# Performance work log

Measured on AMD Instinct MI355X. Metric: run time of the kernel, lower is better.

## Reference

```python
import jax, jax.numpy as jnp
import numpy as np

N = 32768
E = 524288
NFEAT = 256
NHID = 256
NUM_HEADS = 4
HEAD_DIM = NHID // NUM_HEADS
NLAYER = 2
EPS = 1e-5


def setup_inputs():
    keys = iter(jax.random.split(jax.random.key(0), 64))

    def nrm(shape, scale=0.05):
        return jax.random.normal(next(keys), shape, dtype=jnp.float32) * scale

    inp = {
        "x": jax.random.normal(next(keys), (N, NFEAT), dtype=jnp.float32),
        "edge_src": jax.random.randint(next(keys), (E,), 0, N),
        "edge_dst": jax.random.randint(next(keys), (E,), 0, N),
        "edge_attr": jax.random.uniform(next(keys), (E,), dtype=jnp.float32) * 0.1,
        "num_graphs": 64,
    }
    for i in range(NLAYER):
        fin = NFEAT if i == 0 else NHID
        inp["conv_w%d" % i] = nrm((fin, NHID))
        inp["bn_g%d" % i] = jnp.ones((NHID,), jnp.float32)
        inp["bn_b%d" % i] = jnp.zeros((NHID,), jnp.float32)
        inp["bn_m%d" % i] = nrm((NHID,), 0.1)
        inp["bn_v%d" % i] = 1.0 + jax.random.uniform(next(keys), (NHID,), dtype=jnp.float32) * 0.1
        inp["attn_in_w%d" % i] = nrm((3 * NHID, NHID))
        inp["attn_in_b%d" % i] = jnp.zeros((3 * NHID,), jnp.float32)
        inp["attn_out_w%d" % i] = nrm((NHID, NHID))
        inp["attn_out_b%d" % i] = jnp.zeros((NHID,), jnp.float32)
        inp["ln_g%d" % i] = jnp.ones((NHID,), jnp.float32)
        inp["ln_b%d" % i] = jnp.zeros((NHID,), jnp.float32)
    inp["score_w"] = nrm((1, NHID))
    inp["score_b"] = jnp.zeros((1,), jnp.float32)
    return inp


def _mha(xb, iw, ib, ow, ob):
    # torch.nn.MultiheadAttention (batch_first), all graphs same length so
    # key_padding_mask is all-False (no masked positions).
    B, S, H = xb.shape
    q, k, v = jnp.split(xb @ iw.T + ib, 3, axis=-1)
    heads = lambda t: t.reshape(B, S, NUM_HEADS, HEAD_DIM).transpose(0, 2, 1, 3)
    q, k, v = heads(q), heads(k), heads(v)
    scale = jnp.float32(1.0 / np.sqrt(HEAD_DIM))
    att = jax.nn.softmax(jnp.einsum("bhqd,bhkd->bhqk", q, k) * scale, axis=-1)
    o = jnp.einsum("bhqk,bhkd->bhqd", att, v).transpose(0, 2, 1, 3).reshape(B, S, H)
    return o @ ow.T + ob


def _forward(x, edge_attr, params, edge_src, edge_dst, num_graphs):
    n = x.shape[0]
    B = num_graphs
    S = n // B  # equal-sized graphs -> max_nodes == S, pad is a no-op
    h = x
    for i, (cw, bng, bnb, bnm, bnv, iw, ib, ow, ob, lg, lb) in enumerate(params):
        # DIGCNConv: out[dst] += edge_attr * (x @ W)[src]
        conv = jax.ops.segment_sum(edge_attr[:, None] * (h @ cw)[edge_src], edge_dst, num_segments=n)
        # BatchNorm1d (eval mode, running stats)
        conv = (conv - bnm) * jax.lax.rsqrt(bnv + EPS) * bng + bnb
        # ragged gather -> pad/stack -> MHA -> unpad (equal graph sizes => reshape)
        attended = _mha(conv.reshape(B, S, NHID), iw, ib, ow, ob).reshape(n, NHID)
        y = conv + attended
        mu = jnp.mean(y, axis=-1, keepdims=True)
        var = jnp.mean((y - mu) ** 2, axis=-1, keepdims=True)
        h = (y - mu) * jax.lax.rsqrt(var + EPS) * lg + lb  # LayerNorm
        if i < NLAYER - 1:
            h = jax.nn.relu(h)
    return h


def reference(x, edge_src, edge_dst, edge_attr, num_graphs,
              conv_w0, bn_g0, bn_b0, bn_m0, bn_v0, attn_in_w0, attn_in_b0, attn_out_w0, attn_out_b0, ln_g0, ln_b0,
              conv_w1, bn_g1, bn_b1, bn_m1, bn_v1, attn_in_w1, attn_in_b1, attn_out_w1, attn_out_b1, ln_g1, ln_b1,
              score_w, score_b):
    params = [
        (conv_w0, bn_g0, bn_b0, bn_m0, bn_v0, attn_in_w0, attn_in_b0, attn_out_w0, attn_out_b0, ln_g0, ln_b0),
        (conv_w1, bn_g1, bn_b1, bn_m1, bn_v1, attn_in_w1, attn_in_b1, attn_out_w1, attn_out_b1, ln_g1, ln_b1),
    ]
    h = _forward(x, edge_attr, params, edge_src, edge_dst, num_graphs)
    scores = (h @ score_w.T + score_b)[:, 0]
    # emb_list / score_list are per-graph views of these flat arrays
    return h, scores
```

## Files before the change

kernel.cpp:

```cpp
#include <hip/hip_runtime.h>
#include <hip/hip_bf16.h>
#include <math.h>

#define N_NODES 32768
#define E_EDGES 524288
#define NHID    256
#define HEAD_DIM 64
#define SEQ     512
#define EPS_LN  1e-5f
#define SM_SCALE 0.18033688011112042f

typedef __hip_bfloat16 bf16;
typedef __attribute__((ext_vector_type(8))) short short8;
typedef __attribute__((ext_vector_type(4))) float floatx4;
static const size_t NH = (size_t)N_NODES * NHID;

__device__ __forceinline__ void unpack2(unsigned int u, float& lo, float& hi) {
    union { float f; unsigned int i; } a, b;
    a.i = u << 16; b.i = u & 0xffff0000u;
    lo = a.f; hi = b.f;
}

__device__ __forceinline__ void* swzp(void* base, int row, int col) {
    return (char*)base + (((row << 7) + (col << 1)) ^ ((row & 7) << 4));
}

__device__ __forceinline__ void gload16(const bf16* g, void* lds) {
    __builtin_amdgcn_global_load_lds((const __attribute__((address_space(1))) void*)g,
                                     (__attribute__((address_space(3))) void*)lds, 16, 0, 0);
}

__global__ __launch_bounds__(256) void k_stage2(
    const float* __restrict__ cw0, const float* __restrict__ g0, const float* __restrict__ b0,
    const float* __restrict__ m0, const float* __restrict__ v0, const float* __restrict__ iw0,
    const float* __restrict__ ow0,
    const float* __restrict__ cw1, const float* __restrict__ g1, const float* __restrict__ b1,
    const float* __restrict__ m1, const float* __restrict__ v1, const float* __restrict__ iw1,
    const float* __restrict__ ow1,
    bf16* __restrict__ iwb0, bf16* __restrict__ owb0, bf16* __restrict__ cwT0,
    float* __restrict__ bns0, float* __restrict__ bnt0,
    bf16* __restrict__ iwb1, bf16* __restrict__ owb1, bf16* __restrict__ cwT1,
    float* __restrict__ bns1, float* __restrict__ bnt1,
    const float* __restrict__ x, bf16* __restrict__ xb) {
    const int blk = blockIdx.x;
    const int tid = threadIdx.x;
    if (blk >= 1026) {
        size_t i = (size_t)((blk - 1026) * 256 + tid) * 4;
        const float4 v = *(const float4*)(x + i);
        __align__(8) bf16 t4[4];
        t4[0] = __float2bfloat16(v.x);
        t4[1] = __float2bfloat16(v.y);
        t4[2] = __float2bfloat16(v.z);
        t4[3] = __float2bfloat16(v.w);
        *(uint2*)(xb + i) = *(uint2*)t4;
        return;
    }
    const int L = (blk >= 513);
    const int b2 = L ? blk - 513 : blk;
    const float* cw = L ? cw1 : cw0;
    const float* bng = L ? g1 : g0;
    const float* bnb = L ? b1 : b0;
    const float* bnm = L ? m1 : m0;
    const float* bnv = L ? v1 : v0;
    const float* iw = L ? iw1 : iw0;
    const float* ow = L ? ow1 : ow0;
    bf16* iwb = L ? iwb1 : iwb0;
    bf16* owb = L ? owb1 : owb0;
    bf16* cwT = L ? cwT1 : cwT0;
    float* bns = L ? bns1 : bns0;
    float* bnt = L ? bnt1 : bnt0;
    if (b2 < 256) {
        const float* src = (b2 < 192) ? iw : ow;
        bf16* dst = (b2 < 192) ? iwb : owb;
        size_t i = (size_t)((b2 < 192 ? b2 : b2 - 192) * 256 + tid) * 4;
        const float4 v = *(const float4*)(src + i);
        __align__(8) bf16 t4[4];
        t4[0] = __float2bfloat16(v.x);
        t4[1] = __float2bfloat16(v.y);
        t4[2] = __float2bfloat16(v.z);
        t4[3] = __float2bfloat16(v.w);
        *(uint2*)(dst + i) = *(uint2*)t4;
    } else if (b2 < 512) {
        const int k = b2 - 256;
        cwT[(size_t)tid * 256 + k] = __float2bfloat16(cw[(size_t)k * 256 + tid]);
    } else {
        float sv = bng[tid] * rsqrtf(bnv[tid] + EPS_LN);
        bns[tid] = sv;
        bnt[tid] = bnb[tid] - bnm[tid] * sv;
    }
}

__global__ void k_hist(const int* __restrict__ edst, int* __restrict__ counts) {
    int e = blockIdx.x * 256 + threadIdx.x;
    atomicAdd(&counts[edst[e]], 1);
}

__global__ __launch_bounds__(256) void k_scan(const int* __restrict__ counts,
                                              int* __restrict__ offsets,
                                              int* __restrict__ cursor) {
    __shared__ int sums[256];
    const int tid = threadIdx.x;
    const int base = tid * 128;
    int s = 0;
    for (int i = 0; i < 128; ++i) s += counts[base + i];
    sums[tid] = s;
    __syncthreads();
    for (int off = 1; off < 256; off <<= 1) {
        int v = (tid >= off) ? sums[tid - off] : 0;
        __syncthreads();
        sums[tid] += v;
        __syncthreads();
    }
    int run = (tid == 0) ? 0 : sums[tid - 1];
    for (int i = 0; i < 128; ++i) {
        int c = counts[base + i];
        offsets[base + i] = run;
        cursor[base + i] = run;
        run += c;
    }
    if (tid == 255) offsets[32768] = run;
}

__global__ void k_fill(const int* __restrict__ esrc, const int* __restrict__ edst,
                       const float* __restrict__ eattr, int* __restrict__ cursor,
                       int* __restrict__ srcp, float* __restrict__ attrp) {
    int e = blockIdx.x * 256 + threadIdx.x;
    int d = edst[e];
    int slot = atomicAdd(&cursor[d], 1);
    srcp[slot] = esrc[e];
    attrp[slot] = eattr[e];
}

__global__ __launch_bounds__(256) void k_gather(const bf16* __restrict__ t,
                                                const int* __restrict__ offsets,
                                                const int* __restrict__ srcp,
                                                const float* __restrict__ attrp,
                                                const float* __restrict__ bns,
                                                const float* __restrict__ bnt,
                                                bf16* __restrict__ conv) {
    const int node = (blockIdx.x * 256 + threadIdx.x) >> 6;
    const int lane = threadIdx.x & 63;
    const int half = lane >> 5;
    const int l32 = lane & 31;
    const int start = offsets[node];
    const int end = offsets[node + 1];
    float a[8];
#pragma unroll
    for (int i = 0; i < 8; ++i) a[i] = 0.f;
    for (int c0 = start; c0 < end; c0 += 64) {
        const int n = min(64, end - c0);
        int sidx = 0;
        float sa = 0.f;
        if (lane < n) {
            sidx = srcp[c0 + lane];
            sa = attrp[c0 + lane];
        }
        int s = __shfl(sidx, half, 64);
        float aw = __shfl(sa, half, 64);
        uint4 u = *(const uint4*)(t + (size_t)s * 256 + l32 * 8);
        for (int j = 0; j < n; j += 2) {
            const int e2 = (j + 2 + half) & 63;
            const int s2 = __shfl(sidx, e2, 64);
            const float aw2 = __shfl(sa, e2, 64);
            const uint4 u2 = *(const uint4*)(t + (size_t)s2 * 256 + l32 * 8);
            float v0, v1, v2, v3, v4, v5, v6, v7;
            unpack2(u.x, v0, v1);
            unpack2(u.y, v2, v3);
            unpack2(u.z, v4, v5);
            unpack2(u.w, v6, v7);
            a[0] = fmaf(aw, v0, a[0]);
            a[1] = fmaf(aw, v1, a[1]);
            a[2] = fmaf(aw, v2, a[2]);
            a[3] = fmaf(aw, v3, a[3]);
            a[4] = fmaf(aw, v4, a[4]);
            a[5] = fmaf(aw, v5, a[5]);
            a[6] = fmaf(aw, v6, a[6]);
            a[7] = fmaf(aw, v7, a[7]);
            u = u2;
            aw = aw2;
        }
    }
#pragma unroll
    for (int i = 0; i < 8; ++i) a[i] += __shfl_xor(a[i], 32, 64);
    if (half == 0) {
        const int c = l32 * 8;
        const float4 s0 = *(const float4*)(bns + c);
        const float4 s1 = *(const float4*)(bns + c + 4);
        const float4 t0 = *(const float4*)(bnt + c);
        const float4 t1 = *(const float4*)(bnt + c + 4);
        __align__(16) bf16 tmp[8];
        tmp[0] = __float2bfloat16(fmaf(a[0], s0.x, t0.x));
        tmp[1] = __float2bfloat16(fmaf(a[1], s0.y, t0.y));
        tmp[2] = __float2bfloat16(fmaf(a[2], s0.z, t0.z));
        tmp[3] = __float2bfloat16(fmaf(a[3], s0.w, t0.w));
        tmp[4] = __float2bfloat16(fmaf(a[4], s1.x, t1.x));
        tmp[5] = __float2bfloat16(fmaf(a[5], s1.y, t1.y));
        tmp[6] = __float2bfloat16(fmaf(a[6], s1.z, t1.z));
        tmp[7] = __float2bfloat16(fmaf(a[7], s1.w, t1.w));
        *(uint4*)(conv + (size_t)node * 256 + c) = *(uint4*)tmp;
    }
}

__global__ __launch_bounds__(256) void k_gemm(const bf16* __restrict__ A,
                                              const bf16* __restrict__ WT,
                                              const float* __restrict__ bias,
                                              bf16* __restrict__ C, bf16* __restrict__ VT,
                                              int ldc, int qkvmode) {
    __shared__ __align__(16) short As[2][128 * 64];
    __shared__ __align__(16) short Bs[2][128 * 64];
    const int tid = threadIdx.x;
    const int bm = blockIdx.x * 128;
    const int bn = blockIdx.y * 128;
    const int wid = tid >> 6;
    const int lane = tid & 63;
    const int wr = (wid >> 1) * 64;
    const int wc = (wid & 1) * 64;
    const int quad = lane >> 4;
    const int l16 = lane & 15;

    floatx4 acc[4][4];
#pragma unroll
    for (int mi = 0; mi < 4; ++mi)
#pragma unroll
        for (int ni = 0; ni < 4; ++ni)
            acc[mi][ni] = (floatx4){0.f, 0.f, 0.f, 0.f};

    auto STAGE = [&](int ks, int bf) {
#pragma unroll
        for (int t = 0; t < 4; ++t) {
            const int p = ((t * 4 + wid) << 10) + (lane << 4);
            const int row = p >> 7;
            const int cb = (p & 127) ^ ((row & 7) << 4);
            gload16(A + (size_t)(bm + row) * 256 + ks * 64 + (cb >> 1),
                    (char*)&As[bf][0] + ((t * 4 + wid) << 10));
            gload16(WT + (size_t)(bn + row) * 256 + ks * 64 + (cb >> 1),
                    (char*)&Bs[bf][0] + ((t * 4 + wid) << 10));
        }
    };

    STAGE(0, 0);
    __syncthreads();
    for (int t = 0; t < 4; ++t) {
        const int buf = t & 1;
        if (t < 3) STAGE(t + 1, buf ^ 1);
#pragma unroll
        for (int kk = 0; kk < 2; ++kk) {
            const int kcol = kk * 32 + quad * 8;
            short8 af[4], bfr[4];
#pragma unroll
            for (int mi = 0; mi < 4; ++mi)
                af[mi] = *(const short8*)swzp(&As[buf][0], wr + mi * 16 + l16, kcol);
#pragma unroll
            for (int ni = 0; ni < 4; ++ni)
                bfr[ni] = *(const short8*)swzp(&Bs[buf][0], wc + ni * 16 + l16, kcol);
#pragma unroll
            for (int mi = 0; mi < 4; ++mi)
#pragma unroll
                for (int ni = 0; ni < 4; ++ni)
                    acc[mi][ni] = __builtin_amdgcn_mfma_f32_16x16x32_bf16(af[mi], bfr[ni],
                                                                          acc[mi][ni], 0, 0, 0);
        }
        __syncthreads();
    }
    const float cs = (qkvmode && bn < 256) ? SM_SCALE : 1.0f;
    const bool vpath = (qkvmode && bn >= 512);
#pragma unroll
    for (int ni = 0; ni < 4; ++ni) {
        const int gc = bn + wc + ni * 16 + l16;
        const float bv = bias ? bias[gc] : 0.f;
#pragma unroll
        for (int mi = 0; mi < 4; ++mi) {
            const int gr = bm + wr + mi * 16 + quad * 4;
            if (vpath) {
                const int head = (gc - 512) >> 6;
                const int d = (gc - 512) & 63;
                const int bg = gr >> 9;
                const int sl = gr & 511;
                __align__(8) bf16 t4[4];
#pragma unroll
                for (int r = 0; r < 4; ++r) t4[r] = __float2bfloat16(acc[mi][ni][r] + bv);
                *(uint2*)(VT + (((size_t)((bg * 4 + head) * 64 + d)) << 9) + sl) = *(uint2*)t4;
            } else {
#pragma unroll
                for (int r = 0; r < 4; ++r)
                    C[(size_t)(gr + r) * ldc + gc] = __float2bfloat16((acc[mi][ni][r] + bv) * cs);
            }
        }
    }
}

__global__ __launch_bounds__(256) void k_gemmln(const bf16* __restrict__ A,
                                                const bf16* __restrict__ WT,
                                                const float* __restrict__ bias,
                                                const bf16* __restrict__ conv,
                                                const float* __restrict__ lg,
                                                const float* __restrict__ lb,
                                                bf16* __restrict__ h,
                                                const float* __restrict__ sw,
                                                const float* __restrict__ sb,
                                                float* __restrict__ out, int mode) {
    __shared__ __align__(16) short As[2][64 * 64];
    __shared__ __align__(16) short Bs[2][256 * 64];
    const int tid = threadIdx.x;
    const int bm = blockIdx.x * 64;
    const int wid = tid >> 6;
    const int lane = tid & 63;
    const int wc = wid * 64;
    const int quad = lane >> 4;
    const int l16 = lane & 15;

    floatx4 acc[4][4];
#pragma unroll
    for (int mi = 0; mi < 4; ++mi)
#pragma unroll
        for (int ni = 0; ni < 4; ++ni)
            acc[mi][ni] = (floatx4){0.f, 0.f, 0.f, 0.f};

    auto STAGE = [&](int ks, int bf) {
#pragma unroll
        for (int t = 0; t < 2; ++t) {
            const int base = (t * 4 + wid) << 10;
            const int p = base + (lane << 4);
            const int row = p >> 7;
            const int cb = (p & 127) ^ ((row & 7) << 4);
            gload16(A + (size_t)(bm + row) * 256 + ks * 64 + (cb >> 1),
                    (char*)&As[bf][0] + base);
        }
#pragma unroll
        for (int t = 0; t < 8; ++t) {
            const int base = (t * 4 + wid) << 10;
            const int p = base + (lane << 4);
            const int row = p >> 7;
            const int cb = (p & 127) ^ ((row & 7) << 4);
            gload16(WT + (size_t)row * 256 + ks * 64 + (cb >> 1), (char*)&Bs[bf][0] + base);
        }
    };

    STAGE(0, 0);
    __syncthreads();
    for (int t = 0; t < 4; ++t) {
        const int buf = t & 1;
        if (t < 3) STAGE(t + 1, buf ^ 1);
#pragma unroll
        for (int kk = 0; kk < 2; ++kk) {
            const int kcol = kk * 32 + quad * 8;
            short8 af[4], bfr[4];
#pragma unroll
            for (int mi = 0; mi < 4; ++mi)
                af[mi] = *(const short8*)swzp(&As[buf][0], mi * 16 + l16, kcol);
#pragma unroll
            for (int ni = 0; ni < 4; ++ni)
                bfr[ni] = *(const short8*)swzp(&Bs[buf][0], wc + ni * 16 + l16, kcol);
#pragma unroll
            for (int mi = 0; mi < 4; ++mi)
#pragma unroll
                for (int ni = 0; ni < 4; ++ni)
                    acc[mi][ni] = __builtin_amdgcn_mfma_f32_16x16x32_bf16(af[mi], bfr[ni],
                                                                          acc[mi][ni], 0, 0, 0);
        }
        __syncthreads();
    }

#pragma unroll
    for (int ni = 0; ni < 4; ++ni) {
        const int gc = wc + ni * 16 + l16;
        const float bv = bias[gc];
#pragma unroll
        for (int mi = 0; mi < 4; ++mi) {
            const int gr = bm + mi * 16 + quad * 4;
#pragma unroll
            for (int r = 0; r < 4; ++r)
                acc[mi][ni][r] += bv + __bfloat162float(conv[(size_t)(gr + r) * 256 + gc]);
        }
    }

    float* red = (float*)&As[0][0];
    float* red2 = red + 256;
    float* red3 = red2 + 256;
    float* redb = red3 + 256;

#pragma unroll
    for (int mi = 0; mi < 4; ++mi)
#pragma unroll
        for (int r = 0; r < 4; ++r) {
            float s1 = acc[mi][0][r] + acc[mi][1][r] + acc[mi][2][r] + acc[mi][3][r];
            s1 += __shfl_xor(s1, 1, 64);
            s1 += __shfl_xor(s1, 2, 64);
            s1 += __shfl_xor(s1, 4, 64);
            s1 += __shfl_xor(s1, 8, 64);
            if (l16 == 0) red[(mi * 16 + quad * 4 + r) * 4 + wid] = s1;
        }
    float lg4[4], lb4[4], w34[4];
#pragma unroll
    for (int ni = 0; ni < 4; ++ni) {
        const int gc = wc + ni * 16 + l16;
        lg4[ni] = lg[gc];
        lb4[ni] = lb[gc];
        w34[ni] = mode ? lg4[ni] * sw[gc] : 0.f;
    }
    if (mode) {
        float pb = 0.f;
#pragma unroll
        for (int ni = 0; ni < 4; ++ni) pb += lb4[ni] * sw[wc + ni * 16 + l16];
        pb += __shfl_xor(pb, 1, 64);
        pb += __shfl_xor(pb, 2, 64);
        pb += __shfl_xor(pb, 4, 64);
        pb += __shfl_xor(pb, 8, 64);
        if (lane == 0) redb[wid] = pb;
    }
    __syncthreads();

    float mu_[4][4];
#pragma unroll
    for (int mi = 0; mi < 4; ++mi)
#pragma unroll
        for (int r = 0; r < 4; ++r) {
            const int row = mi * 16 + quad * 4 + r;
            const float mu = (red[row * 4 + 0] + red[row * 4 + 1] + red[row * 4 + 2] +
                              red[row * 4 + 3]) * (1.f / 256.f);
            mu_[mi][r] = mu;
            float s2 = 0.f, s3 = 0.f;
#pragma unroll
            for (int ni = 0; ni < 4; ++ni) {
                const float d = acc[mi][ni][r] - mu;
                s2 += d * d;
                s3 += d * w34[ni];
            }
            s2 += __shfl_xor(s2, 1, 64);
            s2 += __shfl_xor(s2, 2, 64);
            s2 += __shfl_xor(s2, 4, 64);
            s2 += __shfl_xor(s2, 8, 64);
            if (mode) {
                s3 += __shfl_xor(s3, 1, 64);
                s3 += __shfl_xor(s3, 2, 64);
                s3 += __shfl_xor(s3, 4, 64);
                s3 += __shfl_xor(s3, 8, 64);
            }
            if (l16 == 0) {
                red2[row * 4 + wid] = s2;
                if (mode) red3[row * 4 + wid] = s3;
            }
        }
    __syncthreads();

    const float B0 = mode ? (redb[0] + redb[1] + redb[2] + redb[3] + sb[0]) : 0.f;
#pragma unroll
    for (int mi = 0; mi < 4; ++mi)
#pragma unroll
        for (int r = 0; r < 4; ++r) {
            const int row = mi * 16 + quad * 4 + r;
            const int gr = bm + row;
            const float mu = mu_[mi][r];
            const float var = (red2[row * 4 + 0] + red2[row * 4 + 1] + red2[row * 4 + 2] +
                               red2[row * 4 + 3]) * (1.f / 256.f);
            const float rstd = rsqrtf(var + EPS_LN);
            if (!mode) {
#pragma unroll
                for (int ni = 0; ni < 4; ++ni) {
                    const int gc = wc + ni * 16 + l16;
                    const float o = fmaf((acc[mi][ni][r] - mu) * rstd, lg4[ni], lb4[ni]);
                    h[(size_t)gr * 256 + gc] = __float2bfloat16(fmaxf(o, 0.f));
                }
            } else {
#pragma unroll
                for (int ni = 0; ni < 4; ++ni) {
                    const int gc = wc + ni * 16 + l16;
                    out[(size_t)gr * 256 + gc] =
                        fmaf((acc[mi][ni][r] - mu) * rstd, lg4[ni], lb4[ni]);
                }
                if (wid == 0 && l16 == 0) {
                    const float S3 = red3[row * 4 + 0] + red3[row * 4 + 1] +
                                     red3[row * 4 + 2] + red3[row * 4 + 3];
                    out[(size_t)N_NODES * 256 + gr] = fmaf(rstd, S3, B0);
                }
            }
        }
}

__global__ __launch_bounds__(256) void k_fattn(const bf16* __restrict__ qkv,
                                               const bf16* __restrict__ vtb,
                                               bf16* __restrict__ ctx) {
    const int bid = ((blockIdx.x & 7) << 8) | (blockIdx.x >> 3);
    const int qt = bid & 7;
    const int head = (bid >> 3) & 3;
    const int b = bid >> 5;
    const int tid = threadIdx.x;
    const int wave = tid >> 6;
    const int lane = tid & 63;
    const int quad = lane >> 4;
    const int l16 = lane & 15;
    const int qrow0 = b * SEQ + qt * 64 + wave * 16;

    __shared__ __align__(16) short Ks[2][64 * 64];
    __shared__ __align__(16) short Vt[2][64 * 64];
    __shared__ __align__(16) short Ps[4][16 * 64];

    const bf16* kbase = qkv + (size_t)(b * SEQ) * 768 + 256 + head * HEAD_DIM;
    const bf16* vbase = vtb + (size_t)((b * 4 + head) * 64) * 512;
    const int pbase = (wave << 10) + (lane << 4);

    short8 af_q[2];
    {
        const bf16* qp = qkv + (size_t)(qrow0 + l16) * 768 + head * HEAD_DIM + quad * 8;
        af_q[0] = *(const short8*)(qp);
        af_q[1] = *(const short8*)(qp + 32);
    }
    short8 ones;
#pragma unroll
    for (int j = 0; j < 8; ++j) ones[j] = (short)0x3F80;

    floatx4 acc[5];
#pragma unroll
    for (int nt = 0; nt < 5; ++nt) acc[nt] = (floatx4){0.f, 0.f, 0.f, 0.f};

    auto STAGE = [&](int kt2, int bf) {
#pragma unroll
        for (int i = 0; i < 2; ++i) {
            const int p = (i << 12) + pbase;
            const int row = p >> 7;
            const int cb = (p & 127) ^ ((row & 7) << 4);
            gload16(kbase + (size_t)(kt2 * 64 + row) * 768 + (cb >> 1),
                    (char*)Ks[bf] + (i << 12) + (wave << 10));
            gload16(vbase + (size_t)row * 512 + kt2 * 64 + (cb >> 1),
                    (char*)Vt[bf] + (i << 12) + (wave << 10));
        }
    };

    STAGE(0, 0);
    __syncthreads();

    for (int kt = 0; kt < 8; ++kt) {
        const int buf = kt & 1;
        if (kt < 7) STAGE(kt + 1, buf ^ 1);

        floatx4 sf[4];
#pragma unroll
        for (int f = 0; f < 4; ++f) {
            const short8 bk0 = *(const short8*)swzp(Ks[buf], f * 16 + l16, quad * 8);
            const short8 bk1 = *(const short8*)swzp(Ks[buf], f * 16 + l16, 32 + quad * 8);
            sf[f] = __builtin_amdgcn_mfma_f32_16x16x32_bf16(af_q[0], bk0,
                                                            (floatx4){0.f, 0.f, 0.f, 0.f}, 0, 0, 0);
            sf[f] = __builtin_amdgcn_mfma_f32_16x16x32_bf16(af_q[1], bk1, sf[f], 0, 0, 0);
        }

        bf16* psb = (bf16*)&Ps[wave][0];
#pragma unroll
        for (int r = 0; r < 4; ++r) {
            const float p0 = exp2f(fminf(sf[0][r], 80.f));
            const float p1 = exp2f(fminf(sf[1][r], 80.f));
            const float p2 = exp2f(fminf(sf[2][r], 80.f));
            const float p3 = exp2f(fminf(sf[3][r], 80.f));
            const int qr = quad * 4 + r;
            *(bf16*)swzp(psb, qr, l16)      = __float2bfloat16(p0);
            *(bf16*)swzp(psb, qr, 16 + l16) = __float2bfloat16(p1);
            *(bf16*)swzp(psb, qr, 32 + l16) = __float2bfloat16(p2);
            *(bf16*)swzp(psb, qr, 48 + l16) = __float2bfloat16(p3);
        }

#pragma unroll
        for (int c2 = 0; c2 < 2; ++c2) {
            const short8 ap = *(const short8*)swzp(psb, l16, c2 * 32 + quad * 8);
#pragma unroll
            for (int nt = 0; nt < 4; ++nt) {
                const short8 bv = *(const short8*)swzp(Vt[buf], nt * 16 + l16, c2 * 32 + quad * 8);
                acc[nt] = __builtin_amdgcn_mfma_f32_16x16x32_bf16(ap, bv, acc[nt], 0, 0, 0);
            }
            acc[4] = __builtin_amdgcn_mfma_f32_16x16x32_bf16(ap, ones, acc[4], 0, 0, 0);
        }
        __syncthreads();
    }

#pragma unroll
    for (int r = 0; r < 4; ++r) {
        const float inv = 1.f / acc[4][r];
        bf16* op = ctx + (size_t)(qrow0 + quad * 4 + r) * 256 + head * HEAD_DIM + l16;
        op[0]  = __float2bfloat16(acc[0][r] * inv);
        op[16] = __float2bfloat16(acc[1][r] * inv);
        op[32] = __float2bfloat16(acc[2][r] * inv);
        op[48] = __float2bfloat16(acc[3][r] * inv);
    }
}

extern "C" void kernel_launch(void* const* d_in, const int* in_sizes, int n_in,
                              void* d_out, int out_size, void* d_ws, size_t ws_size,
                              hipStream_t stream) {
    if (ws_size < (size_t)100663296) return;

    const float* x     = (const float*)d_in[0];
    const int*   esrc  = (const int*)d_in[1];
    const int*   edst  = (const int*)d_in[2];
    const float* eattr = (const float*)d_in[3];

    bf16* convb = (bf16*)d_ws;
    bf16* qkvb  = convb + NH;
    bf16* tb    = qkvb + 3 * NH;
    bf16* vtb   = tb + NH;
    bf16* xb  = qkvb;
    bf16* hb  = qkvb + NH;

    char* scr = (char*)d_out;
    const size_t LBYTES = 393216 + 131072 + 131072 + 2048;
    int*   counts  = (int*)(scr + 2 * LBYTES);
    int*   offsets = counts + 32768;
    int*   cursor  = offsets + 32769;
    int*   srcp    = cursor + 32768;
    float* attrp   = (float*)(srcp + E_EDGES);

    (void)hipMemsetAsync(counts, 0, 32768 * sizeof(int), stream);
    k_hist<<<E_EDGES / 256, 256, 0, stream>>>(edst, counts);
    k_scan<<<1, 256, 0, stream>>>(counts, offsets, cursor);
    k_fill<<<E_EDGES / 256, 256, 0, stream>>>(esrc, edst, eattr, cursor, srcp, attrp);

    bf16*  iwb[2];
    bf16*  owb[2];
    bf16*  cwT[2];
    float* bns[2];
    float* bnt[2];
    for (int L = 0; L < 2; ++L) {
        char* base = scr + (size_t)L * LBYTES;
        iwb[L] = (bf16*)base;
        owb[L] = iwb[L] + 196608;
        cwT[L] = owb[L] + 65536;
        bns[L] = (float*)(cwT[L] + 65536);
        bnt[L] = bns[L] + 256;
    }
    k_stage2<<<9218, 256, 0, stream>>>(
        (const float*)d_in[5], (const float*)d_in[6], (const float*)d_in[7],
        (const float*)d_in[8], (const float*)d_in[9], (const float*)d_in[10],
        (const float*)d_in[12],
        (const float*)d_in[16], (const float*)d_in[17], (const float*)d_in[18],
        (const float*)d_in[19], (const float*)d_in[20], (const float*)d_in[21],
        (const float*)d_in[23],
        iwb[0], owb[0], cwT[0], bns[0], bnt[0],
        iwb[1], owb[1], cwT[1], bns[1], bnt[1],
        x, xb);

    for (int L = 0; L < 2; ++L) {
        int bi = 5 + L * 11;
        const float* ib = (const float*)d_in[bi + 6];
        const float* ob = (const float*)d_in[bi + 8];

        k_gemm<<<dim3(256, 2), 256, 0, stream>>>(L == 0 ? xb : hb, cwT[L], nullptr, tb,
                                                 nullptr, 256, 0);
        k_gather<<<8192, 256, 0, stream>>>(tb, offsets, srcp, attrp, bns[L], bnt[L], convb);
        k_gemm<<<dim3(256, 6), 256, 0, stream>>>(convb, iwb[L], ib, qkvb, vtb, 768, 1);
        k_fattn<<<2048, 256, 0, stream>>>(qkvb, vtb, tb);
        k_gemmln<<<512, 256, 0, stream>>>(tb, owb[L], ob, convb, (const float*)d_in[bi + 9],
                                          (const float*)d_in[bi + 10], hb,
                                          (const float*)d_in[27], (const float*)d_in[28],
                                          (float*)d_out, L);
    }
}
```

Measured before the change: 495.3 us.

## Preload full weight matrix into LDS and reuse row GEMM for conv projection

The GEMM+LayerNorm kernel becomes a general row-block GEMM that loads the entire 256x256 bf16 weight matrix into four LDS buffers up front, then streams only the A tiles double-buffered. It adds a plain-output mode, which replaces the previous tiled k_gemm for the conv weight projection. For the second layer, a small copy kernel first moves the output-projection weights into a scratch buffer. The aim is to stop reloading weight tiles on every k-step. The cost is a large LDS footprint that limits occupancy to about one block per CU, the loss of overlap for weight loads, and an extra kernel launch.

Measured after the change: 528.7 us. +6.7%, slower.

```diff
diff --git a/kernel.cpp b/kernel.cpp
--- a/kernel.cpp
+++ b/kernel.cpp
@@ -289,18 +289,19 @@
     }
 }
 
-__global__ __launch_bounds__(256) void k_gemmln(const bf16* __restrict__ A,
-                                                const bf16* __restrict__ WT,
-                                                const float* __restrict__ bias,
-                                                const bf16* __restrict__ conv,
-                                                const float* __restrict__ lg,
-                                                const float* __restrict__ lb,
-                                                bf16* __restrict__ h,
-                                                const float* __restrict__ sw,
-                                                const float* __restrict__ sb,
-                                                float* __restrict__ out, int mode) {
+__global__ __launch_bounds__(256) void k_rgemm(const bf16* __restrict__ A,
+                                               const bf16* __restrict__ WT,
+                                               const float* __restrict__ bias,
+                                               bf16* __restrict__ C, int ldc,
+                                               const bf16* __restrict__ conv,
+                                               const float* __restrict__ lg,
+                                               const float* __restrict__ lb,
+                                               bf16* __restrict__ h,
+                                               const float* __restrict__ sw,
+                                               const float* __restrict__ sb,
+                                               float* __restrict__ out, int mode) {
+    __shared__ __align__(16) short Bs[4][256 * 64];
     __shared__ __align__(16) short As[2][64 * 64];
-    __shared__ __align__(16) short Bs[2][256 * 64];
     const int tid = threadIdx.x;
     const int bm = blockIdx.x * 64;
     const int wid = tid >> 6;
@@ -316,7 +317,17 @@
         for (int ni = 0; ni < 4; ++ni)
             acc[mi][ni] = (floatx4){0.f, 0.f, 0.f, 0.f};
 
-    auto STAGE = [&](int ks, int bf) {
+#pragma unroll
+    for (int ks = 0; ks < 4; ++ks)
+#pragma unroll
+        for (int t = 0; t < 8; ++t) {
+            const int base = (t * 4 + wid) << 10;
+            const int p = base + (lane << 4);
+            const int row = p >> 7;
+            const int cb = (p & 127) ^ ((row & 7) << 4);
+            gload16(WT + (size_t)row * 256 + ks * 64 + (cb >> 1), (char*)&Bs[ks][0] + base);
+        }
+    auto STAGE_A = [&](int ks, int bf) {
 #pragma unroll
         for (int t = 0; t < 2; ++t) {
             const int base = (t * 4 + wid) << 10;
@@ -326,21 +337,13 @@
             gload16(A + (size_t)(bm + row) * 256 + ks * 64 + (cb >> 1),
                     (char*)&As[bf][0] + base);
         }
-#pragma unroll
-        for (int t = 0; t < 8; ++t) {
-            const int base = (t * 4 + wid) << 10;
-            const int p = base + (lane << 4);
-            const int row = p >> 7;
-            const int cb = (p & 127) ^ ((row & 7) << 4);
-            gload16(WT + (size_t)row * 256 + ks * 64 + (cb >> 1), (char*)&Bs[bf][0] + base);
-        }
     };
-
-    STAGE(0, 0);
+    STAGE_A(0, 0);
     __syncthreads();
-    for (int t = 0; t < 4; ++t) {
-        const int buf = t & 1;
-        if (t < 3) STAGE(t + 1, buf ^ 1);
+
+    for (int ks = 0; ks < 4; ++ks) {
+        const int buf = ks & 1;
+        if (ks < 3) STAGE_A(ks + 1, buf ^ 1);
 #pragma unroll
         for (int kk = 0; kk < 2; ++kk) {
             const int kcol = kk * 32 + quad * 8;
@@ -350,7 +353,7 @@
                 af[mi] = *(const short8*)swzp(&As[buf][0], mi * 16 + l16, kcol);
 #pragma unroll
             for (int ni = 0; ni < 4; ++ni)
-                bfr[ni] = *(const short8*)swzp(&Bs[buf][0], wc + ni * 16 + l16, kcol);
+                bfr[ni] = *(const short8*)swzp(&Bs[ks][0], wc + ni * 16 + l16, kcol);
 #pragma unroll
             for (int mi = 0; mi < 4; ++mi)
 #pragma unroll
@@ -361,6 +364,22 @@
         __syncthreads();
     }
 
+    if (mode == 0) {
+#pragma unroll
+        for (int ni = 0; ni < 4; ++ni) {
+            const int gc = wc + ni * 16 + l16;
+            const float bv = bias ? bias[gc] : 0.f;
+#pragma unroll
+            for (int mi = 0; mi < 4; ++mi) {
+                const int gr = bm + mi * 16 + quad * 4;
+#pragma unroll
+                for (int r = 0; r < 4; ++r)
+                    C[(size_t)(gr + r) * ldc + gc] = __float2bfloat16(acc[mi][ni][r] + bv);
+            }
+        }
+        return;
+    }
+
 #pragma unroll
     for (int ni = 0; ni < 4; ++ni) {
         const int gc = wc + ni * 16 + l16;
@@ -373,7 +392,7 @@
                 acc[mi][ni][r] += bv + __bfloat162float(conv[(size_t)(gr + r) * 256 + gc]);
         }
     }
-
+    const int sc = (mode == 2);
     float* red = (float*)&As[0][0];
     float* red2 = red + 256;
     float* red3 = red2 + 256;
@@ -396,9 +415,9 @@
         const int gc = wc + ni * 16 + l16;
         lg4[ni] = lg[gc];
         lb4[ni] = lb[gc];
-        w34[ni] = mode ? lg4[ni] * sw[gc] : 0.f;
-    }
-    if (mode) {
+        w34[ni] = sc ? lg4[ni] * sw[gc] : 0.f;
+    }
+    if (sc) {
         float pb = 0.f;
 #pragma unroll
         for (int ni = 0; ni < 4; ++ni) pb += lb4[ni] * sw[wc + ni * 16 + l16];
@@ -430,7 +449,7 @@
             s2 += __shfl_xor(s2, 2, 64);
             s2 += __shfl_xor(s2, 4, 64);
             s2 += __shfl_xor(s2, 8, 64);
-            if (mode) {
+            if (sc) {
                 s3 += __shfl_xor(s3, 1, 64);
                 s3 += __shfl_xor(s3, 2, 64);
                 s3 += __shfl_xor(s3, 4, 64);
@@ -438,12 +457,12 @@
             }
             if (l16 == 0) {
                 red2[row * 4 + wid] = s2;
-                if (mode) red3[row * 4 + wid] = s3;
+                if (sc) red3[row * 4 + wid] = s3;
             }
         }
     __syncthreads();
 
-    const float B0 = mode ? (redb[0] + redb[1] + redb[2] + redb[3] + sb[0]) : 0.f;
+    const float B0 = sc ? (redb[0] + redb[1] + redb[2] + redb[3] + sb[0]) : 0.f;
 #pragma unroll
     for (int mi = 0; mi < 4; ++mi)
 #pragma unroll
@@ -454,7 +473,7 @@
             const float var = (red2[row * 4 + 0] + red2[row * 4 + 1] + red2[row * 4 + 2] +
                                red2[row * 4 + 3]) * (1.f / 256.f);
             const float rstd = rsqrtf(var + EPS_LN);
-            if (!mode) {
+            if (!sc) {
 #pragma unroll
                 for (int ni = 0; ni < 4; ++ni) {
                     const int gc = wc + ni * 16 + l16;
@@ -475,6 +494,11 @@
                 }
             }
         }
+}
+
+__global__ void k_copyw(bf16* __restrict__ dst, const bf16* __restrict__ src) {
+    const int i = blockIdx.x * 256 + threadIdx.x;
+    ((uint4*)dst)[i] = ((const uint4*)src)[i];
 }
 
 __global__ __launch_bounds__(256) void k_fattn(const bf16* __restrict__ qkv,
@@ -639,15 +663,24 @@
         int bi = 5 + L * 11;
         const float* ib = (const float*)d_in[bi + 6];
         const float* ob = (const float*)d_in[bi + 8];
-
-        k_gemm<<<dim3(256, 2), 256, 0, stream>>>(L == 0 ? xb : hb, cwT[L], nullptr, tb,
-                                                 nullptr, 256, 0);
+        const float* lgp = (const float*)d_in[bi + 9];
+        const float* lbp = (const float*)d_in[bi + 10];
+
+        k_rgemm<<<512, 256, 0, stream>>>(L == 0 ? xb : hb, cwT[L], nullptr, tb, 256,
+                                         nullptr, nullptr, nullptr, nullptr,
+                                         nullptr, nullptr, nullptr, 0);
         k_gather<<<8192, 256, 0, stream>>>(tb, offsets, srcp, attrp, bns[L], bnt[L], convb);
         k_gemm<<<dim3(256, 6), 256, 0, stream>>>(convb, iwb[L], ib, qkvb, vtb, 768, 1);
         k_fattn<<<2048, 256, 0, stream>>>(qkvb, vtb, tb);
-        k_gemmln<<<512, 256, 0, stream>>>(tb, owb[L], ob, convb, (const float*)d_in[bi + 9],
-                                          (const float*)d_in[bi + 10], hb,
-                                          (const float*)d_in[27], (const float*)d_in[28],
-                                          (float*)d_out, L);
-    }
-}
+        if (L == 0) {
+            k_rgemm<<<512, 256, 0, stream>>>(tb, owb[0], ob, nullptr, 0, convb,
+                                             lgp, lbp, hb, nullptr, nullptr, nullptr, 1);
+        } else {
+            k_copyw<<<32, 256, 0, stream>>>(vtb, owb[1]);
+            k_rgemm<<<512, 256, 0, stream>>>(tb, vtb, ob, nullptr, 0, convb,
+                                             lgp, lbp, nullptr,
+                                             (const float*)d_in[27], (const float*)d_in[28],
+                                             (float*)d_out, 2);
+        }
+    }
+}
```
